# Performance work log

Hardware: AMD Instinct MI355X
Metric: run time of the kernel (lower is better)

The kernel has to match this reference:

```python
import jax, jax.numpy as jnp
import numpy as np

NSITES = 262144
ZP1 = 13  # coordination number Z=12, plus the self row


def setup_inputs() -> dict:
    key = jax.random.key(0)
    k1, k2, k3, k4 = jax.random.split(key, 4)
    In = jax.random.normal(k1, (4, 8, NSITES), dtype=jnp.float32)
    NNsites = jax.random.randint(k2, (ZP1, NSITES), 0, NSITES, dtype=jnp.int32)
    Weights = jax.random.normal(k3, (8, 8, 16), dtype=jnp.float32)  # (K, C_out, 2*C_in)
    bias = jax.random.normal(k4, (8, 8), dtype=jnp.float32)         # (K, C_out)
    return {"In": In, "NNsites": NNsites, "Weights": Weights, "bias": bias}


def reference(In, NNsites, Weights, bias):
    # Original math per neighbor z:
    #   total = concat([In, In[:,:,NN[1+z]]], axis=1)            # (B, 2C_in, N)
    #   o[b,n,k,co] = sum_i W[k,co,i]*total[b,i,n] + bias[k,co]
    #   o summed over channels k, then softplus, accumulated over z.
    # Sum over k commutes with the linear map, so use effective weights.
    C_in = In.shape[1]
    Weff = Weights.sum(axis=0)          # (C_out, 2*C_in)
    beff = bias.sum(axis=0)             # (C_out,)
    Ws, Wn = Weff[:, :C_in], Weff[:, C_in:]
    # self contribution, identical for every z
    self_part = jnp.einsum('oi,bin->bon', Ws, In)          # (B, C_out, N)
    # gather all Z neighbor shells at once: (B, C_in, Z, N)
    neigh = In[:, :, NNsites[1:]]
    neigh_out = jnp.einsum('oi,bizn->bozn', Wn, neigh)     # (B, C_out, Z, N)
    pre = self_part[:, :, None, :] + neigh_out + beff[None, :, None, None]
    return jax.nn.softplus(pre).sum(axis=2)                # (B, C_out, N)
```

## Files before the change

kernel.cpp:

```cpp
#include <hip/hip_runtime.h>
#include <hip/hip_fp16.h>

#define NSITES 262144

struct alignas(16) H8 { __half2 h[4]; };
typedef __attribute__((ext_vector_type(2))) float floatx2;
typedef __attribute__((ext_vector_type(4))) unsigned int uintx4;


__global__ __launch_bounds__(256) void prep_kernel(
    const float* __restrict__ In,
    const float* __restrict__ Weights,
    const float* __restrict__ bias,
    uint2* __restrict__ G8,
    H8*    __restrict__ Sp)
{
    __shared__ float ws[8][8], wn[8][8], be[8];
    int t = threadIdx.x;
    if (t < 64) {
        int o = t >> 3, k = t & 7;
        float s0 = 0.f, s1 = 0.f;
        #pragma unroll
        for (int s = 0; s < 8; ++s) {
            s0 += Weights[s*128 + o*16 + k];
            s1 += Weights[s*128 + o*16 + 8 + k];
        }
        ws[o][k] = s0; wn[o][k] = s1;
    } else if (t < 72) {
        int o = t - 64;
        float s = 0.f;
        #pragma unroll
        for (int q = 0; q < 8; ++q) s += bias[q*8 + o];
        be[o] = s;
    }
    __syncthreads();

    int b    = t & 3;
    int sl   = t >> 2;
    int site = blockIdx.x * 64 + sl;

    float x[8];
    #pragma unroll
    for (int i = 0; i < 8; ++i)
        x[i] = In[(b*8 + i) * NSITES + site];

    float g[8], s[8];
    #pragma unroll
    for (int o = 0; o < 8; ++o) {
        float a0 = 0.f, a1 = be[o];
        #pragma unroll
        for (int i = 0; i < 8; ++i) {
            a0 = fmaf(wn[o][i], x[i], a0);
            a1 = fmaf(ws[o][i], x[i], a1);
        }
        g[o] = a0; s[o] = a1;
    }

    unsigned int w0 = 0, w1 = 0;
    w0 = __builtin_amdgcn_cvt_pk_fp8_f32(g[0], g[1], w0, false);
    w0 = __builtin_amdgcn_cvt_pk_fp8_f32(g[2], g[3], w0, true);
    w1 = __builtin_amdgcn_cvt_pk_fp8_f32(g[4], g[5], w1, false);
    w1 = __builtin_amdgcn_cvt_pk_fp8_f32(g[6], g[7], w1, true);
    G8[site*4 + b] = make_uint2(w0, w1);

    H8 sv;
    #pragma unroll
    for (int p = 0; p < 4; ++p) sv.h[p] = __floats2half2_rn(s[2*p], s[2*p+1]);
    Sp[site*4 + b] = sv;
}

__global__ __launch_bounds__(256) void gather_kernel(
    const H8*    __restrict__ Sp,
    const uint2* __restrict__ G8,
    const int*   __restrict__ NN,
    float*       __restrict__ out)
{
    __shared__ float lds[32][65];
    int t    = threadIdx.x;
    int q    = t & 3;
    int sl   = t >> 2;
    int base = blockIdx.x * 64;
    int n    = base + sl;

    uintx4 spw = __builtin_nontemporal_load((const uintx4*)Sp + (n*4 + q));
    float sp[8];
    #pragma unroll
    for (int p = 0; p < 4; ++p) {
        unsigned int w = spw[p];
        __half2 h; __builtin_memcpy(&h, &w, 4);
        float2 f = __half22float2(h);
        sp[2*p] = f.x; sp[2*p+1] = f.y;
    }

    const float NLOG2E = -1.44269504f;
    float acc[8], prod[8];
    #pragma unroll
    for (int k = 0; k < 8; ++k) { acc[k] = 0.f; prod[k] = 1.f; }

    #pragma unroll
    for (int z = 1; z < 13; ++z) {
        int m = __builtin_nontemporal_load(&NN[z * NSITES + n]);
        uint2 gw = G8[m*4 + q];
        float g[8];
        floatx2 p;
        p = __builtin_amdgcn_cvt_pk_f32_fp8(gw.x, false); g[0]=p[0]; g[1]=p[1];
        p = __builtin_amdgcn_cvt_pk_f32_fp8(gw.x, true ); g[2]=p[0]; g[3]=p[1];
        p = __builtin_amdgcn_cvt_pk_f32_fp8(gw.y, false); g[4]=p[0]; g[5]=p[1];
        p = __builtin_amdgcn_cvt_pk_f32_fp8(gw.y, true ); g[6]=p[0]; g[7]=p[1];
        #pragma unroll
        for (int k = 0; k < 8; ++k) {
            float x  = sp[k] + g[k];
            float ax = fabsf(x);
            acc[k] += fmaxf(x, 0.f);
            float e = __builtin_amdgcn_exp2f(ax * NLOG2E);
            prod[k] = fmaf(prod[k], e, prod[k]);
        }
    }

    #pragma unroll
    for (int k = 0; k < 8; ++k)
        lds[q*8 + k][sl] = acc[k] + 0.69314718f * __builtin_amdgcn_logf(prod[k]);
    __syncthreads();

    int s  = t & 63;
    int j0 = t >> 6;
    #pragma unroll
    for (int r = 0; r < 8; ++r) {
        int j = j0*8 + r;
        __builtin_nontemporal_store(lds[j][s], &out[j * NSITES + base + s]);
    }
}

extern "C" void kernel_launch(void* const* d_in, const int* in_sizes, int n_in,
                              void* d_out, int out_size, void* d_ws, size_t ws_size,
                              hipStream_t stream) {
    const float* In      = (const float*)d_in[0];
    const int*   NN      = (const int*)  d_in[1];
    const float* Weights = (const float*)d_in[2];
    const float* bias    = (const float*)d_in[3];
    float* out = (float*)d_out;

    uint2* G8 = (uint2*)d_ws;
    H8*    Sp = (H8*)((char*)d_ws + (size_t)NSITES * 32);

    prep_kernel<<<NSITES / 64, 256, 0, stream>>>(In, Weights, bias, G8, Sp);
    gather_kernel<<<NSITES / 64, 256, 0, stream>>>(Sp, G8, NN, out);
}
```

Measured before the change: 133.5 us.

## Process two batches per thread with 16-byte gathers and batched index prefetch

Each gather thread now handles two batch slices of a site, so every neighbor fetch becomes one 16-byte load instead of two 8-byte loads, and blocks cover 128 sites. All 12 neighbor indices are loaded up front, and gathers are issued six at a time to increase memory-level parallelism. This doubles per-thread register state (16 accumulators plus six 16-byte buffers), which may reduce occupancy.

```diff
diff --git a/kernel.cpp b/kernel.cpp
--- a/kernel.cpp
+++ b/kernel.cpp
@@ -70,63 +70,79 @@
 }
 
 __global__ __launch_bounds__(256) void gather_kernel(
-    const H8*    __restrict__ Sp,
-    const uint2* __restrict__ G8,
-    const int*   __restrict__ NN,
-    float*       __restrict__ out)
+    const uintx4* __restrict__ Sp4,
+    const uintx4* __restrict__ G16,
+    const int*    __restrict__ NN,
+    float*        __restrict__ out)
 {
-    __shared__ float lds[32][65];
+    __shared__ float lds[32][129];
     int t    = threadIdx.x;
-    int q    = t & 3;
-    int sl   = t >> 2;
-    int base = blockIdx.x * 64;
+    int q    = t & 1;
+    int sl   = t >> 1;
+    int base = blockIdx.x * 128;
     int n    = base + sl;
 
-    uintx4 spw = __builtin_nontemporal_load((const uintx4*)Sp + (n*4 + q));
-    float sp[8];
+    uintx4 sw0 = __builtin_nontemporal_load(Sp4 + n*4 + 2*q);
+    uintx4 sw1 = __builtin_nontemporal_load(Sp4 + n*4 + 2*q + 1);
+    float sp[16];
     #pragma unroll
     for (int p = 0; p < 4; ++p) {
-        unsigned int w = spw[p];
-        __half2 h; __builtin_memcpy(&h, &w, 4);
-        float2 f = __half22float2(h);
-        sp[2*p] = f.x; sp[2*p+1] = f.y;
+        unsigned int wa = sw0[p], wb = sw1[p];
+        __half2 ha, hb;
+        __builtin_memcpy(&ha, &wa, 4);
+        __builtin_memcpy(&hb, &wb, 4);
+        float2 fa = __half22float2(ha), fb = __half22float2(hb);
+        sp[2*p]     = fa.x; sp[2*p+1]     = fa.y;
+        sp[8 + 2*p] = fb.x; sp[8 + 2*p+1] = fb.y;
     }
 
+    int m[12];
+    #pragma unroll
+    for (int z = 0; z < 12; ++z)
+        m[z] = __builtin_nontemporal_load(&NN[(z+1) * NSITES + n]);
+
     const float NLOG2E = -1.44269504f;
-    float acc[8], prod[8];
+    float acc[16], prod[16];
     #pragma unroll
-    for (int k = 0; k < 8; ++k) { acc[k] = 0.f; prod[k] = 1.f; }
+    for (int k = 0; k < 16; ++k) { acc[k] = 0.f; prod[k] = 1.f; }
 
     #pragma unroll
-    for (int z = 1; z < 13; ++z) {
-        int m = __builtin_nontemporal_load(&NN[z * NSITES + n]);
-        uint2 gw = G8[m*4 + q];
-        float g[8];
-        floatx2 p;
-        p = __builtin_amdgcn_cvt_pk_f32_fp8(gw.x, false); g[0]=p[0]; g[1]=p[1];
-        p = __builtin_amdgcn_cvt_pk_f32_fp8(gw.x, true ); g[2]=p[0]; g[3]=p[1];
-        p = __builtin_amdgcn_cvt_pk_f32_fp8(gw.y, false); g[4]=p[0]; g[5]=p[1];
-        p = __builtin_amdgcn_cvt_pk_f32_fp8(gw.y, true ); g[6]=p[0]; g[7]=p[1];
+    for (int zz = 0; zz < 2; ++zz) {
+        uintx4 gw[6];
         #pragma unroll
-        for (int k = 0; k < 8; ++k) {
-            float x  = sp[k] + g[k];
-            float ax = fabsf(x);
-            acc[k] += fmaxf(x, 0.f);
-            float e = __builtin_amdgcn_exp2f(ax * NLOG2E);
-            prod[k] = fmaf(prod[k], e, prod[k]);
+        for (int z = 0; z < 6; ++z)
+            gw[z] = G16[(size_t)m[zz*6 + z] * 2 + q];
+        #pragma unroll
+        for (int z = 0; z < 6; ++z) {
+            float g[16];
+            #pragma unroll
+            for (int p = 0; p < 4; ++p) {
+                floatx2 lo = __builtin_amdgcn_cvt_pk_f32_fp8(gw[z][p], false);
+                floatx2 hi = __builtin_amdgcn_cvt_pk_f32_fp8(gw[z][p], true);
+                g[4*p]   = lo[0]; g[4*p+1] = lo[1];
+                g[4*p+2] = hi[0]; g[4*p+3] = hi[1];
+            }
+            #pragma unroll
+            for (int k = 0; k < 16; ++k) {
+                float x  = sp[k] + g[k];
+                float ax = fabsf(x);
+                acc[k] += fmaxf(x, 0.f);
+                float e = __builtin_amdgcn_exp2f(ax * NLOG2E);
+                prod[k] = fmaf(prod[k], e, prod[k]);
+            }
         }
     }
 
     #pragma unroll
-    for (int k = 0; k < 8; ++k)
-        lds[q*8 + k][sl] = acc[k] + 0.69314718f * __builtin_amdgcn_logf(prod[k]);
+    for (int k = 0; k < 16; ++k)
+        lds[q*16 + k][sl] = acc[k] + 0.69314718f * __builtin_amdgcn_logf(prod[k]);
     __syncthreads();
 
-    int s  = t & 63;
-    int j0 = t >> 6;
+    int s  = t & 127;
+    int j0 = t >> 7;
     #pragma unroll
-    for (int r = 0; r < 8; ++r) {
-        int j = j0*8 + r;
+    for (int r = 0; r < 16; ++r) {
+        int j = j0*16 + r;
         __builtin_nontemporal_store(lds[j][s], &out[j * NSITES + base + s]);
     }
 }
@@ -140,9 +156,11 @@
     const float* bias    = (const float*)d_in[3];
     float* out = (float*)d_out;
 
-    uint2* G8 = (uint2*)d_ws;
-    H8*    Sp = (H8*)((char*)d_ws + (size_t)NSITES * 32);
+    uint2*  G8  = (uint2*)d_ws;
+    H8*     Sp  = (H8*)((char*)d_ws + (size_t)NSITES * 32);
+    uintx4* G16 = (uintx4*)G8;
+    uintx4* Sp4 = (uintx4*)Sp;
 
     prep_kernel<<<NSITES / 64, 256, 0, stream>>>(In, Weights, bias, G8, Sp);
-    gather_kernel<<<NSITES / 64, 256, 0, stream>>>(Sp, G8, NN, out);
+    gather_kernel<<<NSITES / 128, 256, 0, stream>>>(Sp4, G16, NN, out);
 }
```

Result: slower. 138.3 us (+3.6%).
